# Performance work log

Hardware: AMD Instinct MI355X
Metric: run time of the kernel (lower is better)

The kernel has to match this reference:

```python
import jax, jax.numpy as jnp
import numpy as np

B, T, C, H, HS = 64, 128, 4096, 32, 128  # T must equal HS = C // H (source code constraint)
SCALE = 32.0 ** -0.5  # fixed constant in source, NOT head_size**-0.5


def setup_inputs() -> dict:
    key = jax.random.key(0)
    ks = jax.random.split(key, 6)
    s = 0.02
    return {
        "x": jax.random.normal(ks[0], (B, T, C), dtype=jnp.float32),
        "wq": jax.random.normal(ks[1], (H, C, HS), dtype=jnp.float32) * s,
        "wk": jax.random.normal(ks[2], (H, C, HS), dtype=jnp.float32) * s,
        "wv": jax.random.normal(ks[3], (H, C, HS), dtype=jnp.float32) * s,
        "wp": jax.random.normal(ks[4], (C, C), dtype=jnp.float32) * s,
        "bp": jnp.zeros((C,), dtype=jnp.float32),
    }


def reference(x, wq, wk, wv, wp, bp):
    # Batched per-head projections (source loops over heads; math identical).
    q = jnp.einsum("btc,hcs->bhts", x, wq)  # [B,H,T,HS]
    k = jnp.einsum("btc,hcs->bhts", x, wk)
    v = jnp.einsum("btc,hcs->bhts", x, wv)
    wei = jnp.einsum("bhts,bhus->bhtu", q, k) * SCALE  # [B,H,Tq,Tk]
    # Source uses F.softmax(wei, dim=1) on [B,Tq,Tk] -> softmax over QUERY axis.
    wei = jax.nn.softmax(wei, axis=2)
    out = jnp.einsum("bhtu,bhus->bhts", wei, v)  # [B,H,T,HS]
    # torch.cat(dim=1) over heads -> [B, H*T, HS]; then transpose(1,2) -> [B, HS, H*T]
    out = out.reshape(B, H * T, HS).transpose(0, 2, 1)  # [B, HS, H*T]; H*T == C
    out = jnp.einsum("bse,oe->bso", out, wp) + bp  # proj Linear
    return out  # dropout is identity in eval mode
```

## Files before the change

### kernel.cpp

```cpp
#include <hip/hip_runtime.h>
#include <cstddef>
#include <cstdint>

#define NB 64
#define NH 32
#define NT 128
#define NHS 128
#define NC 4096
#define SCALE 0.17677669529663687f
#define SLD 136

typedef __bf16 bf16_t;
typedef __bf16 bf16x8 __attribute__((ext_vector_type(8)));
typedef float  f32x4  __attribute__((ext_vector_type(4)));

__device__ __forceinline__ void load_lds16(const bf16_t* g, bf16_t* l) {
    __builtin_amdgcn_global_load_lds(
        (const __attribute__((address_space(1))) char*)g,
        (__attribute__((address_space(3))) char*)l,
        16, 0, 0);
}

__global__ __launch_bounds__(256) void cvt_bf16_kernel(
    const float* __restrict__ in, bf16_t* __restrict__ out, int n8)
{
    int i = blockIdx.x * 256 + threadIdx.x;
    if (i >= n8) return;
    const float4* p = (const float4*)in + (size_t)i * 2;
    float4 a = p[0], b = p[1];
    bf16x8 o;
    o[0] = (bf16_t)a.x; o[1] = (bf16_t)a.y; o[2] = (bf16_t)a.z; o[3] = (bf16_t)a.w;
    o[4] = (bf16_t)b.x; o[5] = (bf16_t)b.y; o[6] = (bf16_t)b.z; o[7] = (bf16_t)b.w;
    ((bf16x8*)out)[i] = o;
}

__global__ __launch_bounds__(256) void cvt_w_transpose_kernel(
    const float* __restrict__ wq, const float* __restrict__ wk, const float* __restrict__ wv,
    bf16_t* __restrict__ qt, bf16_t* __restrict__ kt, bf16_t* __restrict__ vt)
{
    const float* w; bf16_t* o;
    if (blockIdx.y == 0)      { w = wq; o = qt; }
    else if (blockIdx.y == 1) { w = wk; o = kt; }
    else                      { w = wv; o = vt; }
    const int h   = blockIdx.x >> 7;
    const int rem = blockIdx.x & 127;
    const int c0  = (rem >> 1) * 64;
    const int s0  = (rem & 1) * 64;
    const float* W = w + (size_t)h * NC * NHS;
    bf16_t* O = o + (size_t)h * NHS * NC;

    __shared__ float t[64][65];
    const int tid = threadIdx.x;
    #pragma unroll
    for (int it = 0; it < 16; ++it) {
        int idx = it * 256 + tid;
        int r = idx >> 6, cc = idx & 63;
        t[r][cc] = W[(size_t)(c0 + r) * NHS + s0 + cc];
    }
    __syncthreads();
    #pragma unroll
    for (int it = 0; it < 16; ++it) {
        int idx = it * 256 + tid;
        int sr = idx >> 6, cr = idx & 63;
        O[(size_t)(s0 + sr) * NC + c0 + cr] = (bf16_t)t[cr][sr];
    }
}

__device__ __forceinline__ void gemm128x128(
    const bf16_t* __restrict__ A, const bf16_t* __restrict__ BT,
    int ldA, int ldBT, f32x4 acc[4][4])
{
    __shared__ __align__(16) bf16_t As[128 * 32];
    __shared__ __align__(16) bf16_t Bs[128 * 32];

    const int tid  = threadIdx.x;
    const int lane = tid & 63;
    const int wave = tid >> 6;
    const int wr = (wave >> 1) * 64;
    const int wc = (wave & 1) * 64;
    const int srow = tid >> 2;
    const int scol = (tid & 3) * 8;
    const int m0 = wr + (lane & 15);
    const int n0 = wc + (lane & 15);
    const int kq = (lane >> 4) * 8;

    for (int k0 = 0; k0 < NC; k0 += 32) {
        load_lds16(A  + (size_t)srow        * ldA  + k0 + scol, &As[srow * 32 + scol]);
        load_lds16(A  + (size_t)(srow + 64) * ldA  + k0 + scol, &As[(srow + 64) * 32 + scol]);
        load_lds16(BT + (size_t)srow        * ldBT + k0 + scol, &Bs[srow * 32 + scol]);
        load_lds16(BT + (size_t)(srow + 64) * ldBT + k0 + scol, &Bs[(srow + 64) * 32 + scol]);
        __syncthreads();

        bf16x8 af[4], bfr[4];
        #pragma unroll
        for (int i = 0; i < 4; ++i) af[i]  = *(const bf16x8*)&As[(m0 + i * 16) * 32 + kq];
        #pragma unroll
        for (int j = 0; j < 4; ++j) bfr[j] = *(const bf16x8*)&Bs[(n0 + j * 16) * 32 + kq];
        #pragma unroll
        for (int i = 0; i < 4; ++i)
            #pragma unroll
            for (int j = 0; j < 4; ++j)
                acc[i][j] = __builtin_amdgcn_mfma_f32_16x16x32_bf16(af[i], bfr[j], acc[i][j], 0, 0, 0);
        __syncthreads();
    }
}

__global__ __launch_bounds__(256) void qkv_mfma_kernel(
    const bf16_t* __restrict__ x,
    const bf16_t* __restrict__ wqT, const bf16_t* __restrict__ wkT, const bf16_t* __restrict__ wvT,
    bf16_t* __restrict__ q, bf16_t* __restrict__ k, bf16_t* __restrict__ v)
{
    const int bh = blockIdx.x;
    const int b = bh >> 5, h = bh & 31;
    const bf16_t* wT; bf16_t* o;
    if (blockIdx.y == 0)      { wT = wqT; o = q; }
    else if (blockIdx.y == 1) { wT = wkT; o = k; }
    else                      { wT = wvT; o = v; }

    const bf16_t* A  = x  + (size_t)b * NT * NC;
    const bf16_t* BT = wT + (size_t)h * NHS * NC;
    bf16_t* D = o + (size_t)bh * NT * NHS;

    f32x4 acc[4][4] = {};
    gemm128x128(A, BT, NC, NC, acc);

    const int lane = threadIdx.x & 63;
    const int wave = threadIdx.x >> 6;
    const int wr = (wave >> 1) * 64;
    const int wc = (wave & 1) * 64;
    const int rbase = wr + (lane >> 4) * 4;
    const int col  = wc + (lane & 15);
    if (blockIdx.y == 2) {
        #pragma unroll
        for (int i = 0; i < 4; ++i)
            #pragma unroll
            for (int j = 0; j < 4; ++j)
                #pragma unroll
                for (int r = 0; r < 4; ++r)
                    D[(size_t)(col + j * 16) * NT + rbase + i * 16 + r] = (bf16_t)acc[i][j][r];
    } else {
        #pragma unroll
        for (int i = 0; i < 4; ++i)
            #pragma unroll
            for (int j = 0; j < 4; ++j)
                #pragma unroll
                for (int r = 0; r < 4; ++r)
                    D[(size_t)(rbase + i * 16 + r) * NHS + col + j * 16] = (bf16_t)acc[i][j][r];
    }
}

__global__ __launch_bounds__(256) void attn_mfma_kernel(
    const bf16_t* __restrict__ q, const bf16_t* __restrict__ k,
    const bf16_t* __restrict__ vT, bf16_t* __restrict__ attnT)
{
    __shared__ __align__(16) bf16_t As[128 * 32];
    __shared__ __align__(16) bf16_t Bs[128 * 32];
    __shared__ __align__(16) bf16_t S[NT * SLD];

    const int bh = blockIdx.x;
    const int b = bh >> 5, h = bh & 31;
    const bf16_t* Q  = q  + (size_t)bh * NT * NHS;
    const bf16_t* K  = k  + (size_t)bh * NT * NHS;
    const bf16_t* VT = vT + (size_t)bh * NT * NHS;

    const int tid  = threadIdx.x;
    const int lane = tid & 63;
    const int wave = tid >> 6;
    const int wr = (wave >> 1) * 64;
    const int wc = (wave & 1) * 64;
    const int srow = tid >> 2;
    const int scol = (tid & 3) * 8;
    const int m0 = wr + (lane & 15);
    const int n0 = wc + (lane & 15);
    const int kq = (lane >> 4) * 8;
    const int rbase = wr + (lane >> 4) * 4;

    f32x4 acc[4][4] = {};

    for (int k0 = 0; k0 < NHS; k0 += 32) {
        load_lds16(Q + (size_t)srow        * NHS + k0 + scol, &As[srow * 32 + scol]);
        load_lds16(Q + (size_t)(srow + 64) * NHS + k0 + scol, &As[(srow + 64) * 32 + scol]);
        load_lds16(K + (size_t)srow        * NHS + k0 + scol, &Bs[srow * 32 + scol]);
        load_lds16(K + (size_t)(srow + 64) * NHS + k0 + scol, &Bs[(srow + 64) * 32 + scol]);
        __syncthreads();
        bf16x8 af[4], bfr[4];
        #pragma unroll
        for (int i = 0; i < 4; ++i) af[i]  = *(const bf16x8*)&As[(m0 + i * 16) * 32 + kq];
        #pragma unroll
        for (int j = 0; j < 4; ++j) bfr[j] = *(const bf16x8*)&Bs[(n0 + j * 16) * 32 + kq];
        #pragma unroll
        for (int i = 0; i < 4; ++i)
            #pragma unroll
            for (int j = 0; j < 4; ++j)
                acc[i][j] = __builtin_amdgcn_mfma_f32_16x16x32_bf16(af[i], bfr[j], acc[i][j], 0, 0, 0);
        __syncthreads();
    }
    #pragma unroll
    for (int i = 0; i < 4; ++i)
        #pragma unroll
        for (int j = 0; j < 4; ++j)
            #pragma unroll
            for (int r = 0; r < 4; ++r)
                S[(rbase + i * 16 + r) * SLD + wc + j * 16 + (lane & 15)] =
                    (bf16_t)(acc[i][j][r] * SCALE);
    __syncthreads();

    if (tid < NT) {
        const int u = tid;
        float m = -1e30f;
        for (int t = 0; t < NT; ++t) m = fmaxf(m, (float)S[t * SLD + u]);
        float sum = 0.f;
        for (int t = 0; t < NT; ++t) sum += __expf((float)S[t * SLD + u] - m);
        const float inv = 1.0f / sum;
        for (int t = 0; t < NT; ++t)
            S[t * SLD + u] = (bf16_t)(__expf((float)S[t * SLD + u] - m) * inv);
    }
    __syncthreads();

    #pragma unroll
    for (int i = 0; i < 4; ++i)
        #pragma unroll
        for (int j = 0; j < 4; ++j)
            acc[i][j] = (f32x4)(0.0f);

    for (int k0 = 0; k0 < NT; k0 += 32) {
        load_lds16(VT + (size_t)srow        * NT + k0 + scol, &As[srow * 32 + scol]);
        load_lds16(VT + (size_t)(srow + 64) * NT + k0 + scol, &As[(srow + 64) * 32 + scol]);
        __syncthreads();
        bf16x8 af[4], bfr[4];
        #pragma unroll
        for (int i = 0; i < 4; ++i) af[i]  = *(const bf16x8*)&As[(m0 + i * 16) * 32 + kq];
        #pragma unroll
        for (int j = 0; j < 4; ++j) bfr[j] = *(const bf16x8*)&S[(n0 + j * 16) * SLD + k0 + kq];
        #pragma unroll
        for (int i = 0; i < 4; ++i)
            #pragma unroll
            for (int j = 0; j < 4; ++j)
                acc[i][j] = __builtin_amdgcn_mfma_f32_16x16x32_bf16(af[i], bfr[j], acc[i][j], 0, 0, 0);
        __syncthreads();
    }
    bf16_t* AT = attnT + (size_t)b * NHS * NC + h * NT;
    #pragma unroll
    for (int i = 0; i < 4; ++i)
        #pragma unroll
        for (int j = 0; j < 4; ++j)
            #pragma unroll
            for (int r = 0; r < 4; ++r)
                AT[(size_t)(rbase + i * 16 + r) * NC + wc + j * 16 + (lane & 15)] =
                    (bf16_t)acc[i][j][r];
}

__global__ __launch_bounds__(256) void proj_mfma_kernel(
    const bf16_t* __restrict__ attnT, const bf16_t* __restrict__ wpb,
    const float* __restrict__ bp, float* __restrict__ out)
{
    const int b  = blockIdx.x;
    const int o0 = blockIdx.y * 128;
    const bf16_t* A  = attnT + (size_t)b * NHS * NC;
    const bf16_t* BT = wpb + (size_t)o0 * NC;

    f32x4 acc[4][4] = {};
    gemm128x128(A, BT, NC, NC, acc);

    float* D = out + (size_t)b * NHS * NC + o0;
    const int lane = threadIdx.x & 63;
    const int wave = threadIdx.x >> 6;
    const int wr = (wave >> 1) * 64;
    const int wc = (wave & 1) * 64;
    const int rbase = wr + (lane >> 4) * 4;
    #pragma unroll
    for (int i = 0; i < 4; ++i)
        #pragma unroll
        for (int j = 0; j < 4; ++j) {
            const int n = wc + j * 16 + (lane & 15);
            const float bias = bp[o0 + n];
            #pragma unroll
            for (int r = 0; r < 4; ++r)
                D[(size_t)(rbase + i * 16 + r) * NC + n] = acc[i][j][r] + bias;
        }
}

extern "C" void kernel_launch(void* const* d_in, const int* in_sizes, int n_in,
                              void* d_out, int out_size, void* d_ws, size_t ws_size,
                              hipStream_t stream) {
    const float* x  = (const float*)d_in[0];
    const float* wq = (const float*)d_in[1];
    const float* wk = (const float*)d_in[2];
    const float* wv = (const float*)d_in[3];
    const float* wp = (const float*)d_in[4];
    const float* bp = (const float*)d_in[5];
    float* out = (float*)d_out;

    const size_t NX = (size_t)NB * NT * NC;
    const size_t NW = (size_t)NH * NC * NHS;
    bf16_t* xb  = (bf16_t*)d_ws;
    bf16_t* wqT = xb  + NX;
    bf16_t* wkT = wqT + NW;
    bf16_t* wvT = wkT + NW;
    bf16_t* wpb = wvT + NW;
    bf16_t* qb  = wpb + NW;
    bf16_t* kb  = qb  + NX;
    bf16_t* vb  = kb  + NX;
    bf16_t* atT = vb  + NX;

    cvt_bf16_kernel<<<(int)(NX / 8 / 256), 256, 0, stream>>>(x, xb, (int)(NX / 8));
    cvt_w_transpose_kernel<<<dim3(4096, 3), 256, 0, stream>>>(wq, wk, wv, wqT, wkT, wvT);
    cvt_bf16_kernel<<<(int)(NW / 8 / 256), 256, 0, stream>>>(wp, wpb, (int)(NW / 8));

    qkv_mfma_kernel<<<dim3(NB * NH, 3), 256, 0, stream>>>(xb, wqT, wkT, wvT, qb, kb, vb);
    attn_mfma_kernel<<<NB * NH, 256, 0, stream>>>(qb, kb, vb, atT);
    proj_mfma_kernel<<<dim3(NB, 32), 256, 0, stream>>>(atT, wpb, bp, out);
}
```

Baseline: 1.692 ms.

## Replace 128x128 GEMMs with pipelined 256x256 double-buffered MFMA GEMM core

Replaces the simple 128x128 GEMM tile used by the QKV and projection kernels with a 256x256, 512-thread tile. It uses a 64-wide K step, double-buffered LDS with an XOR swizzle, and staggered prefetch using explicit waitcnt, barriers and setprio. The QKV GEMM now treats the three weight tensors as one concatenated N=12288 matrix and uses an XCD-aware block remap, relying on wqT/wkT/wvT being contiguous in the workspace. The goal is more operand reuse and overlap of global loads with MFMA work. In exchange it uses more registers and LDS per block, and the hand-tuned synchronisation is fragile.

```diff
diff --git a/kernel.cpp b/kernel.cpp
--- a/kernel.cpp
+++ b/kernel.cpp
@@ -66,87 +66,199 @@
     }
 }
 
-__device__ __forceinline__ void gemm128x128(
-    const bf16_t* __restrict__ A, const bf16_t* __restrict__ BT,
-    int ldA, int ldBT, f32x4 acc[4][4])
-{
-    __shared__ __align__(16) bf16_t As[128 * 32];
-    __shared__ __align__(16) bf16_t Bs[128 * 32];
+#define TILE_EL 16384
+
+__device__ __forceinline__ void gemm256_core(
+    const bf16_t* __restrict__ A, const bf16_t* __restrict__ BT, f32x4 acc[8][4])
+{
+    __shared__ __align__(16) bf16_t As[2 * TILE_EL];
+    __shared__ __align__(16) bf16_t Bs[2 * TILE_EL];
 
     const int tid  = threadIdx.x;
     const int lane = tid & 63;
-    const int wave = tid >> 6;
-    const int wr = (wave >> 1) * 64;
-    const int wc = (wave & 1) * 64;
-    const int srow = tid >> 2;
-    const int scol = (tid & 3) * 8;
-    const int m0 = wr + (lane & 15);
-    const int n0 = wc + (lane & 15);
-    const int kq = (lane >> 4) * 8;
-
-    for (int k0 = 0; k0 < NC; k0 += 32) {
-        load_lds16(A  + (size_t)srow        * ldA  + k0 + scol, &As[srow * 32 + scol]);
-        load_lds16(A  + (size_t)(srow + 64) * ldA  + k0 + scol, &As[(srow + 64) * 32 + scol]);
-        load_lds16(BT + (size_t)srow        * ldBT + k0 + scol, &Bs[srow * 32 + scol]);
-        load_lds16(BT + (size_t)(srow + 64) * ldBT + k0 + scol, &Bs[(srow + 64) * 32 + scol]);
-        __syncthreads();
-
-        bf16x8 af[4], bfr[4];
-        #pragma unroll
-        for (int i = 0; i < 4; ++i) af[i]  = *(const bf16x8*)&As[(m0 + i * 16) * 32 + kq];
-        #pragma unroll
-        for (int j = 0; j < 4; ++j) bfr[j] = *(const bf16x8*)&Bs[(n0 + j * 16) * 32 + kq];
-        #pragma unroll
-        for (int i = 0; i < 4; ++i)
-            #pragma unroll
-            for (int j = 0; j < 4; ++j)
-                acc[i][j] = __builtin_amdgcn_mfma_f32_16x16x32_bf16(af[i], bfr[j], acc[i][j], 0, 0, 0);
-        __syncthreads();
-    }
-}
-
-__global__ __launch_bounds__(256) void qkv_mfma_kernel(
-    const bf16_t* __restrict__ x,
-    const bf16_t* __restrict__ wqT, const bf16_t* __restrict__ wkT, const bf16_t* __restrict__ wvT,
+    const int w    = tid >> 6;
+    const int wr   = w >> 2;
+    const int wc   = w & 3;
+
+    const int srow  = tid >> 3;
+    const int scol  = ((tid & 7) * 8) ^ (((tid >> 3) & 7) << 3);
+    const int sslot = tid * 8;
+
+    const int frow = lane & 15;
+    const int fk   = (lane >> 4) * 8;
+    int aoff[2][2][4];
+    #pragma unroll
+    for (int ks = 0; ks < 2; ++ks)
+        #pragma unroll
+        for (int mh = 0; mh < 2; ++mh)
+            #pragma unroll
+            for (int q = 0; q < 4; ++q) {
+                int r = wr * 128 + mh * 64 + q * 16 + frow;
+                aoff[ks][mh][q] = r * 64 + ((ks * 32 + fk) ^ ((r & 7) << 3));
+            }
+    int boff[2][4];
+    #pragma unroll
+    for (int ks = 0; ks < 2; ++ks)
+        #pragma unroll
+        for (int n = 0; n < 4; ++n) {
+            int r = wc * 64 + n * 16 + frow;
+            boff[ks][n] = r * 64 + ((ks * 32 + fk) ^ ((r & 7) << 3));
+        }
+
+    auto stage = [&](const bf16_t* __restrict__ G, int half, int k0, bf16_t* dst) {
+        #pragma unroll
+        for (int jj = 0; jj < 2; ++jj) {
+            const int j = half * 2 + jj;
+            load_lds16(G + (size_t)(j * 64 + srow) * NC + (k0 + scol),
+                       dst + j * 4096 + sslot);
+        }
+    };
+
+    stage(A,  0, 0, As);           stage(A,  1, 0, As);
+    stage(BT, 0, 0, Bs);           stage(BT, 1, 0, Bs);
+    stage(A,  0, 64, As + TILE_EL); stage(A,  1, 64, As + TILE_EL);
+    stage(BT, 0, 64, Bs + TILE_EL); stage(BT, 1, 64, Bs + TILE_EL);
+    asm volatile("s_waitcnt vmcnt(8)" ::: "memory");
+    __builtin_amdgcn_s_barrier();
+    __builtin_amdgcn_sched_barrier(0);
+
+    for (int t = 0; t < NC / 64; ++t) {
+        bf16_t* Ac = As + (t & 1) * TILE_EL;
+        bf16_t* Bc = Bs + (t & 1) * TILE_EL;
+        const int  kn = t * 64 + 128;
+        const bool pf = (t < NC / 64 - 2);
+
+        bf16x8 b0[4], b1[4], a[4];
+        #pragma unroll
+        for (int n = 0; n < 4; ++n) b0[n] = *(const bf16x8*)(Bc + boff[0][n]);
+        #pragma unroll
+        for (int n = 0; n < 4; ++n) b1[n] = *(const bf16x8*)(Bc + boff[1][n]);
+        #pragma unroll
+        for (int q = 0; q < 4; ++q) a[q] = *(const bf16x8*)(Ac + aoff[0][0][q]);
+        __builtin_amdgcn_s_setprio(1);
+        #pragma unroll
+        for (int q = 0; q < 4; ++q)
+            #pragma unroll
+            for (int n = 0; n < 4; ++n)
+                acc[q][n] = __builtin_amdgcn_mfma_f32_16x16x32_bf16(a[q], b0[n], acc[q][n], 0, 0, 0);
+        __builtin_amdgcn_s_setprio(0);
+        asm volatile("s_waitcnt lgkmcnt(0)" ::: "memory");
+        __builtin_amdgcn_s_barrier();
+        __builtin_amdgcn_sched_barrier(0);
+
+        if (pf) stage(BT, 0, kn, Bc);
+        #pragma unroll
+        for (int q = 0; q < 4; ++q) a[q] = *(const bf16x8*)(Ac + aoff[0][1][q]);
+        __builtin_amdgcn_s_setprio(1);
+        #pragma unroll
+        for (int q = 0; q < 4; ++q)
+            #pragma unroll
+            for (int n = 0; n < 4; ++n)
+                acc[4 + q][n] = __builtin_amdgcn_mfma_f32_16x16x32_bf16(a[q], b0[n], acc[4 + q][n], 0, 0, 0);
+        __builtin_amdgcn_s_setprio(0);
+
+        if (pf) stage(BT, 1, kn, Bc);
+        #pragma unroll
+        for (int q = 0; q < 4; ++q) a[q] = *(const bf16x8*)(Ac + aoff[1][0][q]);
+        __builtin_amdgcn_s_setprio(1);
+        #pragma unroll
+        for (int q = 0; q < 4; ++q)
+            #pragma unroll
+            for (int n = 0; n < 4; ++n)
+                acc[q][n] = __builtin_amdgcn_mfma_f32_16x16x32_bf16(a[q], b1[n], acc[q][n], 0, 0, 0);
+        __builtin_amdgcn_s_setprio(0);
+
+        #pragma unroll
+        for (int q = 0; q < 4; ++q) a[q] = *(const bf16x8*)(Ac + aoff[1][1][q]);
+        __builtin_amdgcn_s_setprio(1);
+        #pragma unroll
+        for (int q = 0; q < 4; ++q)
+            #pragma unroll
+            for (int n = 0; n < 4; ++n)
+                acc[4 + q][n] = __builtin_amdgcn_mfma_f32_16x16x32_bf16(a[q], b1[n], acc[4 + q][n], 0, 0, 0);
+        __builtin_amdgcn_s_setprio(0);
+
+        asm volatile("s_waitcnt lgkmcnt(0)" ::: "memory");
+        __builtin_amdgcn_s_barrier();
+        __builtin_amdgcn_sched_barrier(0);
+        if (pf) {
+            stage(A, 0, kn, Ac); stage(A, 1, kn, Ac);
+            asm volatile("s_waitcnt vmcnt(8)" ::: "memory");
+        } else if (t == NC / 64 - 2) {
+            asm volatile("s_waitcnt vmcnt(0)" ::: "memory");
+        }
+        __builtin_amdgcn_s_barrier();
+        __builtin_amdgcn_sched_barrier(0);
+    }
+}
+
+__global__ __launch_bounds__(512, 2) void qkv_gemm256_kernel(
+    const bf16_t* __restrict__ xb, const bf16_t* __restrict__ wcat,
     bf16_t* __restrict__ q, bf16_t* __restrict__ k, bf16_t* __restrict__ v)
 {
-    const int bh = blockIdx.x;
-    const int b = bh >> 5, h = bh & 31;
-    const bf16_t* wT; bf16_t* o;
-    if (blockIdx.y == 0)      { wT = wqT; o = q; }
-    else if (blockIdx.y == 1) { wT = wkT; o = k; }
-    else                      { wT = wvT; o = v; }
-
-    const bf16_t* A  = x  + (size_t)b * NT * NC;
-    const bf16_t* BT = wT + (size_t)h * NHS * NC;
-    bf16_t* D = o + (size_t)bh * NT * NHS;
-
-    f32x4 acc[4][4] = {};
-    gemm128x128(A, BT, NC, NC, acc);
-
-    const int lane = threadIdx.x & 63;
-    const int wave = threadIdx.x >> 6;
-    const int wr = (wave >> 1) * 64;
-    const int wc = (wave & 1) * 64;
-    const int rbase = wr + (lane >> 4) * 4;
-    const int col  = wc + (lane & 15);
-    if (blockIdx.y == 2) {
-        #pragma unroll
-        for (int i = 0; i < 4; ++i)
-            #pragma unroll
-            for (int j = 0; j < 4; ++j)
-                #pragma unroll
-                for (int r = 0; r < 4; ++r)
-                    D[(size_t)(col + j * 16) * NT + rbase + i * 16 + r] = (bf16_t)acc[i][j][r];
-    } else {
-        #pragma unroll
-        for (int i = 0; i < 4; ++i)
-            #pragma unroll
-            for (int j = 0; j < 4; ++j)
-                #pragma unroll
-                for (int r = 0; r < 4; ++r)
-                    D[(size_t)(rbase + i * 16 + r) * NHS + col + j * 16] = (bf16_t)acc[i][j][r];
-    }
+    const int bid = blockIdx.x;
+    const int wg  = (bid & 7) * 192 + (bid >> 3);
+    const int mt  = wg / 48;
+    const int nt  = wg - mt * 48;
+    const int Mb  = mt << 8;
+    const int Nb  = nt << 8;
+
+    f32x4 acc[8][4] = {};
+    gemm256_core(xb + (size_t)Mb * NC, wcat + (size_t)Nb * NC, acc);
+
+    const int tid = threadIdx.x, lane = tid & 63, w = tid >> 6;
+    const int wr = w >> 2, wc = w & 3;
+    const int tens = Nb >> 12;
+    bf16_t* const outp = (tens == 0) ? q : (tens == 1) ? k : v;
+    const int colb = Nb + wc * 64 + (lane & 15);
+    const int rowb = Mb + wr * 128 + ((lane >> 4) << 2);
+    #pragma unroll
+    for (int i = 0; i < 8; ++i)
+        #pragma unroll
+        for (int r = 0; r < 4; ++r) {
+            const int m  = rowb + i * 16 + r;
+            const int bb = m >> 7, tt = m & 127;
+            #pragma unroll
+            for (int n = 0; n < 4; ++n) {
+                const int ng = colb + n * 16;
+                const int hh = (ng >> 7) & 31, ss = ng & 127;
+                const size_t base = (size_t)((bb << 5) + hh) << 14;
+                if (tens == 2) outp[base + ss * NT  + tt] = (bf16_t)acc[i][n][r];
+                else           outp[base + tt * NHS + ss] = (bf16_t)acc[i][n][r];
+            }
+        }
+}
+
+__global__ __launch_bounds__(512, 2) void proj_gemm256_kernel(
+    const bf16_t* __restrict__ attnT, const bf16_t* __restrict__ wpb,
+    const float* __restrict__ bp, float* __restrict__ out)
+{
+    const int bid = blockIdx.x;
+    const int wg  = (bid & 7) * 64 + (bid >> 3);
+    const int mt  = wg >> 4;
+    const int nt  = wg & 15;
+    const int Mb  = mt << 8;
+    const int Nb  = nt << 8;
+
+    f32x4 acc[8][4] = {};
+    gemm256_core(attnT + (size_t)Mb * NC, wpb + (size_t)Nb * NC, acc);
+
+    const int tid = threadIdx.x, lane = tid & 63, w = tid >> 6;
+    const int wr = w >> 2, wc = w & 3;
+    const int colb = Nb + wc * 64 + (lane & 15);
+    const int rowb = Mb + wr * 128 + ((lane >> 4) << 2);
+    float bias[4];
+    #pragma unroll
+    for (int n = 0; n < 4; ++n) bias[n] = bp[colb + n * 16];
+    #pragma unroll
+    for (int i = 0; i < 8; ++i)
+        #pragma unroll
+        for (int r = 0; r < 4; ++r) {
+            const size_t m = (size_t)(rowb + i * 16 + r);
+            #pragma unroll
+            for (int n = 0; n < 4; ++n)
+                out[m * NC + colb + n * 16] = acc[i][n][r] + bias[n];
+        }
 }
 
 __global__ __launch_bounds__(256) void attn_mfma_kernel(
@@ -250,36 +362,6 @@
                     (bf16_t)acc[i][j][r];
 }
 
-__global__ __launch_bounds__(256) void proj_mfma_kernel(
-    const bf16_t* __restrict__ attnT, const bf16_t* __restrict__ wpb,
-    const float* __restrict__ bp, float* __restrict__ out)
-{
-    const int b  = blockIdx.x;
-    const int o0 = blockIdx.y * 128;
-    const bf16_t* A  = attnT + (size_t)b * NHS * NC;
-    const bf16_t* BT = wpb + (size_t)o0 * NC;
-
-    f32x4 acc[4][4] = {};
-    gemm128x128(A, BT, NC, NC, acc);
-
-    float* D = out + (size_t)b * NHS * NC + o0;
-    const int lane = threadIdx.x & 63;
-    const int wave = threadIdx.x >> 6;
-    const int wr = (wave >> 1) * 64;
-    const int wc = (wave & 1) * 64;
-    const int rbase = wr + (lane >> 4) * 4;
-    #pragma unroll
-    for (int i = 0; i < 4; ++i)
-        #pragma unroll
-        for (int j = 0; j < 4; ++j) {
-            const int n = wc + j * 16 + (lane & 15);
-            const float bias = bp[o0 + n];
-            #pragma unroll
-            for (int r = 0; r < 4; ++r)
-                D[(size_t)(rbase + i * 16 + r) * NC + n] = acc[i][j][r] + bias;
-        }
-}
-
 extern "C" void kernel_launch(void* const* d_in, const int* in_sizes, int n_in,
                               void* d_out, int out_size, void* d_ws, size_t ws_size,
                               hipStream_t stream) {
@@ -307,7 +389,7 @@
     cvt_w_transpose_kernel<<<dim3(4096, 3), 256, 0, stream>>>(wq, wk, wv, wqT, wkT, wvT);
     cvt_bf16_kernel<<<(int)(NW / 8 / 256), 256, 0, stream>>>(wp, wpb, (int)(NW / 8));
 
-    qkv_mfma_kernel<<<dim3(NB * NH, 3), 256, 0, stream>>>(xb, wqT, wkT, wvT, qb, kb, vb);
+    qkv_gemm256_kernel<<<1536, 512, 0, stream>>>(xb, wqT, qb, kb, vb);
     attn_mfma_kernel<<<NB * NH, 256, 0, stream>>>(qb, kb, vb, atT);
-    proj_mfma_kernel<<<dim3(NB, 32), 256, 0, stream>>>(atT, wpb, bp, out);
-}
+    proj_gemm256_kernel<<<512, 512, 0, stream>>>(atT, wpb, bp, out);
+}
```

Result: faster. 1.648 ms (-2.6%).
